# Kernel optimization log

Hardware: AMD Instinct MI355X
Metric: run time of the kernel (lower is better)

The kernel has to match this reference:

```python
import jax, jax.numpy as jnp
import numpy as np

EPS = 1e-6  # F.cosine_similarity eps


def setup_inputs() -> dict:
    key = jax.random.key(0)
    kx, = jax.random.split(key, 1)
    N, M, D = 1024, 32, 256
    x = jax.random.normal(kx, (N, M, D), dtype=jnp.float32)
    w = jnp.array([10.0], dtype=jnp.float32)  # init_w
    b = jnp.array([-5.0], dtype=jnp.float32)  # init_b
    return {"x": x, "w": w, "b": b}


def _ge2e_softmax_loss(x, w, b):
    N, M, D = x.shape
    # centroids over all utterances of each speaker: (N, D)
    cent = x.mean(axis=1)
    # modified centroid excluding utterance i (used when k == j): (N, M, D)
    mod_cent = (x.sum(axis=1, keepdims=True) - x) / (M - 1)

    x_norm = jnp.linalg.norm(x, axis=-1)          # (N, M)
    cent_norm = jnp.linalg.norm(cent, axis=-1)    # (N,)
    mod_norm = jnp.linalg.norm(mod_cent, axis=-1) # (N, M)

    # off-diagonal cosine sim via one batched matmul: (N, M, N)
    dots = jnp.einsum('nmd,kd->nmk', x, cent)
    sim = dots / jnp.maximum(x_norm[:, :, None] * cent_norm[None, None, :], EPS)

    # diagonal (k == j) uses the modified centroid: (N, M)
    diag_sim = jnp.sum(x * mod_cent, axis=-1) / jnp.maximum(x_norm * mod_norm, EPS)

    # splice modified-centroid sims onto the k == j diagonal
    eye = jnp.eye(N, dtype=bool)[:, None, :]  # (N, 1, N)
    S = jnp.where(eye, diag_sim[:, :, None], sim)  # (N, M, N)

    calc = w[0] * S + b[0]
    # L = -S_{ji,j} + logsumexp_k S_{ji,k}
    diag_calc = w[0] * diag_sim + b[0]
    loss = (-diag_calc + jax.nn.logsumexp(calc, axis=-1)).sum()
    return loss


def reference(x, w, b):
    return _ge2e_softmax_loss(x, w, b)
```

## Files before the change

kernel.cpp:

```cpp
#include <hip/hip_runtime.h>
#include <hip/hip_bf16.h>
#include <math.h>

typedef float f32x4 __attribute__((ext_vector_type(4)));
typedef short short8 __attribute__((ext_vector_type(8)));

#define GEPS 1e-6f

static __device__ __forceinline__ short8 ldb8(const __hip_bfloat16* p) {
  return *reinterpret_cast<const short8*>(p);
}

__global__ __launch_bounds__(256) void k1_prep(
    const float* __restrict__ x,
    __hip_bfloat16* __restrict__ xhg, __hip_bfloat16* __restrict__ xlg,
    __hip_bfloat16* __restrict__ chg, __hip_bfloat16* __restrict__ clg,
    float* __restrict__ invcn, float* __restrict__ xn, float* __restrict__ dsim)
{
  const int n = blockIdx.x;
  const int tid = threadIdx.x;
  const int lane = tid & 63;
  const int wv = tid >> 6;
  __shared__ float xsh[32 * 256];
  __shared__ float sl[256];
  __shared__ float red[4];

  const float* xg = x + (size_t)n * 8192;
  float s = 0.f;
  #pragma unroll
  for (int m = 0; m < 32; ++m) {
    float v = xg[m * 256 + tid];
    xsh[m * 256 + tid] = v;
    s += v;
    __hip_bfloat16 h = __float2bfloat16(v);
    float hf = __bfloat162float(h);
    xhg[(size_t)n * 8192 + m * 256 + tid] = h;
    xlg[(size_t)n * 8192 + m * 256 + tid] = __float2bfloat16(v - hf);
  }
  sl[tid] = s;
  const float c = s * 0.03125f;
  {
    __hip_bfloat16 h = __float2bfloat16(c);
    float hf = __bfloat162float(h);
    chg[n * 256 + tid] = h;
    clg[n * 256 + tid] = __float2bfloat16(c - hf);
  }
  float c2 = c * c;
  #pragma unroll
  for (int off = 32; off; off >>= 1) c2 += __shfl_xor(c2, off, 64);
  if (lane == 0) red[wv] = c2;
  __syncthreads();
  if (tid == 0) invcn[n] = 1.0f / sqrtf(red[0] + red[1] + red[2] + red[3]);

  #pragma unroll
  for (int g = 0; g < 8; ++g) {
    const int m = wv + 4 * g;
    float a1 = 0.f, a2 = 0.f, a3 = 0.f;
    #pragma unroll
    for (int e = 0; e < 4; ++e) {
      const int d = lane + 64 * e;
      const float xv = xsh[m * 256 + d];
      const float mo = (sl[d] - xv) / 31.0f;
      a1 += xv * xv;
      a2 += xv * mo;
      a3 += mo * mo;
    }
    #pragma unroll
    for (int off = 32; off; off >>= 1) {
      a1 += __shfl_xor(a1, off, 64);
      a2 += __shfl_xor(a2, off, 64);
      a3 += __shfl_xor(a3, off, 64);
    }
    if (lane == 0) {
      const float xnv = sqrtf(a1);
      const float mn  = sqrtf(a3);
      xn[n * 32 + m]   = xnv;
      dsim[n * 32 + m] = a2 / fmaxf(xnv * mn, GEPS);
    }
  }
}

__global__ __launch_bounds__(256, 2) void k2_mfma(
    const __hip_bfloat16* __restrict__ xhg, const __hip_bfloat16* __restrict__ xlg,
    const __hip_bfloat16* __restrict__ chg, const __hip_bfloat16* __restrict__ clg,
    const float* __restrict__ invcn, const float* __restrict__ xn,
    const float* __restrict__ dsim, const float* __restrict__ wp,
    const float* __restrict__ bp, float* __restrict__ out)
{
  const int bid = blockIdx.x;
  const int tid = threadIdx.x;
  const int wv = tid >> 6;
  const int lane = tid & 63;
  const int q = lane >> 4;
  const int l15 = lane & 15;
  const int rowbase = bid * 64;

  __shared__ float rs[64];
  if (tid < 64) rs[tid] = 0.f;
  __syncthreads();

  const float w = wp[0], b = bp[0];
  const float B = fabsf(w) + fabsf(b);
  const float L2E = 1.44269504088896f;
  const float u = (b - B) * L2E;
  const float wl = w * L2E;

  float srow[4][4], er[4][4];
  #pragma unroll
  for (int mt = 0; mt < 4; ++mt)
    #pragma unroll
    for (int r = 0; r < 4; ++r) {
      const int grow = rowbase + mt * 16 + q * 4 + r;
      srow[mt][r] = wl / xn[grow];
      er[mt][r]   = fmaf(dsim[grow], wl, u);
    }

  float S[4][4];
  #pragma unroll
  for (int mt = 0; mt < 4; ++mt)
    #pragma unroll
    for (int r = 0; r < 4; ++r) S[mt][r] = 0.f;

  #pragma unroll 1
  for (int ci = 0; ci < 2; ++ci) {
    const int ct = wv * 2 + ci;
    const int colbase = ct * 128;
    f32x4 acc[4][8];
    #pragma unroll
    for (int mt = 0; mt < 4; ++mt)
      #pragma unroll
      for (int kt = 0; kt < 8; ++kt) acc[mt][kt] = (f32x4){0.f, 0.f, 0.f, 0.f};

    #pragma unroll 1
    for (int ck = 0; ck < 8; ++ck) {
      const int d0 = ck * 32 + q * 8;
      short8 a_h[4], a_l[4];
      #pragma unroll
      for (int mt = 0; mt < 4; ++mt) {
        const size_t abase = (size_t)(rowbase + mt * 16 + l15) * 256 + d0;
        a_h[mt] = ldb8(xhg + abase);
        a_l[mt] = ldb8(xlg + abase);
      }
      #pragma unroll
      for (int kt = 0; kt < 8; ++kt) {
        const size_t bbase = (size_t)(colbase + kt * 16 + l15) * 256 + d0;
        const short8 b_h = ldb8(chg + bbase);
        const short8 b_l = ldb8(clg + bbase);
        #pragma unroll
        for (int mt = 0; mt < 4; ++mt) {
          acc[mt][kt] = __builtin_amdgcn_mfma_f32_16x16x32_bf16(a_l[mt], b_h, acc[mt][kt], 0, 0, 0);
          acc[mt][kt] = __builtin_amdgcn_mfma_f32_16x16x32_bf16(a_h[mt], b_l, acc[mt][kt], 0, 0, 0);
          acc[mt][kt] = __builtin_amdgcn_mfma_f32_16x16x32_bf16(a_h[mt], b_h, acc[mt][kt], 0, 0, 0);
        }
      }
    }

    #pragma unroll
    for (int kt = 0; kt < 8; ++kt) {
      const int colg = colbase + kt * 16 + l15;
      const float tc = invcn[colg];
      #pragma unroll
      for (int mt = 0; mt < 4; ++mt) {
        const int nrow = (rowbase + mt * 16) >> 5;
        #pragma unroll
        for (int r = 0; r < 4; ++r) {
          float p = exp2f(fmaf(acc[mt][kt][r] * srow[mt][r], tc, u));
          if (colg == nrow) p = exp2f(er[mt][r]);
          S[mt][r] += p;
        }
      }
    }
  }

  #pragma unroll
  for (int mt = 0; mt < 4; ++mt)
    #pragma unroll
    for (int r = 0; r < 4; ++r) {
      float v = S[mt][r];
      v += __shfl_xor(v, 1, 64);
      v += __shfl_xor(v, 2, 64);
      v += __shfl_xor(v, 4, 64);
      v += __shfl_xor(v, 8, 64);
      if (l15 == 0) atomicAdd(&rs[mt * 16 + q * 4 + r], v);
    }
  __syncthreads();

  if (tid < 64) {
    const int grow = rowbase + tid;
    float lr = -fmaf(w, dsim[grow], b) + B + log2f(rs[tid]) * 0.6931471805599453f;
    #pragma unroll
    for (int off = 1; off < 64; off <<= 1) lr += __shfl_xor(lr, off, 64);
    if (tid == 0) atomicAdd(out, lr);
  }
}

extern "C" void kernel_launch(void* const* d_in, const int* in_sizes, int n_in,
                              void* d_out, int out_size, void* d_ws, size_t ws_size,
                              hipStream_t stream)
{
  const float* x = (const float*)d_in[0];
  const float* w = (const float*)d_in[1];
  const float* b = (const float*)d_in[2];
  float* out = (float*)d_out;

  char* W = (char*)d_ws;
  __hip_bfloat16* xhg = (__hip_bfloat16*)(W);
  __hip_bfloat16* xlg = (__hip_bfloat16*)(W + 16777216);
  __hip_bfloat16* chg = (__hip_bfloat16*)(W + 33554432);
  __hip_bfloat16* clg = (__hip_bfloat16*)(W + 34078720);
  float* invcn = (float*)(W + 34603008);
  float* xn    = (float*)(W + 34607104);
  float* dsim  = (float*)(W + 34738176);
  hipMemsetAsync(out, 0, sizeof(float), stream);
  k1_prep<<<1024, 256, 0, stream>>>(x, xhg, xlg, chg, clg, invcn, xn, dsim);
  k2_mfma<<<512, 256, 0, stream>>>(xhg, xlg, chg, clg, invcn, xn, dsim, w, b, out);
}
```

Before: 200.0 us.

## Split column range across blocks, vectorize prep, add final reduction kernel

The MFMA kernel now assigns each block a 64-row by 256-column tile instead of all 1024 columns. That gives 2048 blocks with smaller accumulators and allows occupancy of 3 blocks per CU. Partial row sums go to a global buffer via atomics, and a new third kernel computes the log and the final reduction. The prep kernel is vectorized to float4 loads and derives the modified-centroid norms algebraically without shared-memory staging. In exchange, A tiles are reloaded by four blocks, and the change adds an extra memset and an extra kernel launch.

```diff
diff --git a/kernel.cpp b/kernel.cpp
--- a/kernel.cpp
+++ b/kernel.cpp
@@ -7,71 +7,84 @@
 
 #define GEPS 1e-6f
 
-static __device__ __forceinline__ short8 ldb8(const __hip_bfloat16* p) {
+static __device__ __forceinline__ short8 ldb8(const unsigned short* p) {
   return *reinterpret_cast<const short8*>(p);
+}
+
+static __device__ __forceinline__ void bfsplit(float v, unsigned short& h, unsigned short& l) {
+  __hip_bfloat16 hb = __float2bfloat16(v);
+  h = *reinterpret_cast<unsigned short*>(&hb);
+  float r = v - __bfloat162float(hb);
+  __hip_bfloat16 lb = __float2bfloat16(r);
+  l = *reinterpret_cast<unsigned short*>(&lb);
 }
 
 __global__ __launch_bounds__(256) void k1_prep(
     const float* __restrict__ x,
-    __hip_bfloat16* __restrict__ xhg, __hip_bfloat16* __restrict__ xlg,
-    __hip_bfloat16* __restrict__ chg, __hip_bfloat16* __restrict__ clg,
+    unsigned short* __restrict__ xhg, unsigned short* __restrict__ xlg,
+    unsigned short* __restrict__ chg, unsigned short* __restrict__ clg,
     float* __restrict__ invcn, float* __restrict__ xn, float* __restrict__ dsim)
 {
   const int n = blockIdx.x;
   const int tid = threadIdx.x;
-  const int lane = tid & 63;
-  const int wv = tid >> 6;
-  __shared__ float xsh[32 * 256];
-  __shared__ float sl[256];
-  __shared__ float red[4];
-
-  const float* xg = x + (size_t)n * 8192;
-  float s = 0.f;
-  #pragma unroll
-  for (int m = 0; m < 32; ++m) {
-    float v = xg[m * 256 + tid];
-    xsh[m * 256 + tid] = v;
-    s += v;
-    __hip_bfloat16 h = __float2bfloat16(v);
-    float hf = __bfloat162float(h);
-    xhg[(size_t)n * 8192 + m * 256 + tid] = h;
-    xlg[(size_t)n * 8192 + m * 256 + tid] = __float2bfloat16(v - hf);
-  }
-  sl[tid] = s;
-  const float c = s * 0.03125f;
-  {
-    __hip_bfloat16 h = __float2bfloat16(c);
-    float hf = __bfloat162float(h);
-    chg[n * 256 + tid] = h;
-    clg[n * 256 + tid] = __float2bfloat16(c - hf);
-  }
-  float c2 = c * c;
-  #pragma unroll
-  for (int off = 32; off; off >>= 1) c2 += __shfl_xor(c2, off, 64);
-  if (lane == 0) red[wv] = c2;
-  __syncthreads();
-  if (tid == 0) invcn[n] = 1.0f / sqrtf(red[0] + red[1] + red[2] + red[3]);
-
-  #pragma unroll
-  for (int g = 0; g < 8; ++g) {
-    const int m = wv + 4 * g;
-    float a1 = 0.f, a2 = 0.f, a3 = 0.f;
-    #pragma unroll
-    for (int e = 0; e < 4; ++e) {
-      const int d = lane + 64 * e;
-      const float xv = xsh[m * 256 + d];
-      const float mo = (sl[d] - xv) / 31.0f;
-      a1 += xv * xv;
-      a2 += xv * mo;
-      a3 += mo * mo;
-    }
+  const int c4 = tid & 63;
+  const int mq = tid >> 6;
+  __shared__ f32x4 part[4][64];
+
+  f32x4 xr[8];
+  f32x4 ps = (f32x4){0.f, 0.f, 0.f, 0.f};
+  const size_t nbase = (size_t)n * 8192;
+
+  #pragma unroll
+  for (int p = 0; p < 8; ++p) {
+    const int m = mq * 8 + p;
+    const size_t off = nbase + m * 256 + c4 * 4;
+    f32x4 v = *reinterpret_cast<const f32x4*>(x + off);
+    xr[p] = v;
+    ps += v;
+    ushort4 hv, lv;
+    bfsplit(v.x, hv.x, lv.x);
+    bfsplit(v.y, hv.y, lv.y);
+    bfsplit(v.z, hv.z, lv.z);
+    bfsplit(v.w, hv.w, lv.w);
+    *reinterpret_cast<ushort4*>(xhg + off) = hv;
+    *reinterpret_cast<ushort4*>(xlg + off) = lv;
+  }
+  part[mq][c4] = ps;
+  __syncthreads();
+
+  f32x4 sl = part[0][c4] + part[1][c4] + part[2][c4] + part[3][c4];
+
+  if (mq == 0) {
+    f32x4 c = sl * 0.03125f;
+    ushort4 hv, lv;
+    bfsplit(c.x, hv.x, lv.x);
+    bfsplit(c.y, hv.y, lv.y);
+    bfsplit(c.z, hv.z, lv.z);
+    bfsplit(c.w, hv.w, lv.w);
+    *reinterpret_cast<ushort4*>(chg + n * 256 + c4 * 4) = hv;
+    *reinterpret_cast<ushort4*>(clg + n * 256 + c4 * 4) = lv;
+  }
+
+  float s2 = sl.x * sl.x + sl.y * sl.y + sl.z * sl.z + sl.w * sl.w;
+  #pragma unroll
+  for (int off = 32; off; off >>= 1) s2 += __shfl_xor(s2, off, 64);
+  if (tid == 0) invcn[n] = 32.0f / sqrtf(s2);
+
+  #pragma unroll
+  for (int p = 0; p < 8; ++p) {
+    const f32x4 v = xr[p];
+    float a1 = v.x * v.x + v.y * v.y + v.z * v.z + v.w * v.w;
+    float sx = v.x * sl.x + v.y * sl.y + v.z * sl.z + v.w * sl.w;
     #pragma unroll
     for (int off = 32; off; off >>= 1) {
       a1 += __shfl_xor(a1, off, 64);
-      a2 += __shfl_xor(a2, off, 64);
-      a3 += __shfl_xor(a3, off, 64);
-    }
-    if (lane == 0) {
+      sx += __shfl_xor(sx, off, 64);
+    }
+    if (c4 == 0) {
+      const int m = mq * 8 + p;
+      const float a2 = (sx - a1) * (1.0f / 31.0f);
+      const float a3 = (s2 - 2.0f * sx + a1) * (1.0f / 961.0f);
       const float xnv = sqrtf(a1);
       const float mn  = sqrtf(a3);
       xn[n * 32 + m]   = xnv;
@@ -80,24 +93,65 @@
   }
 }
 
-__global__ __launch_bounds__(256, 2) void k2_mfma(
-    const __hip_bfloat16* __restrict__ xhg, const __hip_bfloat16* __restrict__ xlg,
-    const __hip_bfloat16* __restrict__ chg, const __hip_bfloat16* __restrict__ clg,
+__global__ __launch_bounds__(256, 3) void k2_mfma(
+    const unsigned short* __restrict__ xhg, const unsigned short* __restrict__ xlg,
+    const unsigned short* __restrict__ chg, const unsigned short* __restrict__ clg,
     const float* __restrict__ invcn, const float* __restrict__ xn,
     const float* __restrict__ dsim, const float* __restrict__ wp,
-    const float* __restrict__ bp, float* __restrict__ out)
+    const float* __restrict__ bp, float* __restrict__ row_sum)
 {
   const int bid = blockIdx.x;
+  const int rowbase = (bid >> 2) * 64;
+  const int cq = bid & 3;
   const int tid = threadIdx.x;
   const int wv = tid >> 6;
   const int lane = tid & 63;
   const int q = lane >> 4;
   const int l15 = lane & 15;
-  const int rowbase = bid * 64;
+  const int colbase = cq * 256 + wv * 64;
 
   __shared__ float rs[64];
   if (tid < 64) rs[tid] = 0.f;
   __syncthreads();
+
+  f32x4 acc[4][4];
+  #pragma unroll
+  for (int mt = 0; mt < 4; ++mt)
+    #pragma unroll
+    for (int kt = 0; kt < 4; ++kt) acc[mt][kt] = (f32x4){0.f, 0.f, 0.f, 0.f};
+
+  #pragma unroll 1
+  for (int ck = 0; ck < 8; ++ck) {
+    const int d0 = ck * 32 + q * 8;
+    short8 a_h[4], a_l[4], b_h[4], b_l[4];
+    #pragma unroll
+    for (int mt = 0; mt < 4; ++mt) {
+      const size_t abase = (size_t)(rowbase + mt * 16 + l15) * 256 + d0;
+      a_h[mt] = ldb8(xhg + abase);
+      a_l[mt] = ldb8(xlg + abase);
+    }
+    #pragma unroll
+    for (int kt = 0; kt < 4; ++kt) {
+      const size_t bbase = (size_t)(colbase + kt * 16 + l15) * 256 + d0;
+      b_h[kt] = ldb8(chg + bbase);
+      b_l[kt] = ldb8(clg + bbase);
+    }
+    #pragma unroll
+    for (int mt = 0; mt < 4; ++mt)
+      #pragma unroll
+      for (int kt = 0; kt < 4; ++kt)
+        acc[mt][kt] = __builtin_amdgcn_mfma_f32_16x16x32_bf16(a_l[mt], b_h[kt], acc[mt][kt], 0, 0, 0);
+    #pragma unroll
+    for (int mt = 0; mt < 4; ++mt)
+      #pragma unroll
+      for (int kt = 0; kt < 4; ++kt)
+        acc[mt][kt] = __builtin_amdgcn_mfma_f32_16x16x32_bf16(a_h[mt], b_l[kt], acc[mt][kt], 0, 0, 0);
+    #pragma unroll
+    for (int mt = 0; mt < 4; ++mt)
+      #pragma unroll
+      for (int kt = 0; kt < 4; ++kt)
+        acc[mt][kt] = __builtin_amdgcn_mfma_f32_16x16x32_bf16(a_h[mt], b_h[kt], acc[mt][kt], 0, 0, 0);
+  }
 
   const float w = wp[0], b = bp[0];
   const float B = fabsf(w) + fabsf(b);
@@ -105,93 +159,49 @@
   const float u = (b - B) * L2E;
   const float wl = w * L2E;
 
-  float srow[4][4], er[4][4];
-  #pragma unroll
-  for (int mt = 0; mt < 4; ++mt)
+  #pragma unroll
+  for (int mt = 0; mt < 4; ++mt) {
+    const int nrow = (rowbase + mt * 16) >> 5;
     #pragma unroll
     for (int r = 0; r < 4; ++r) {
       const int grow = rowbase + mt * 16 + q * 4 + r;
-      srow[mt][r] = wl / xn[grow];
-      er[mt][r]   = fmaf(dsim[grow], wl, u);
-    }
-
-  float S[4][4];
-  #pragma unroll
-  for (int mt = 0; mt < 4; ++mt)
-    #pragma unroll
-    for (int r = 0; r < 4; ++r) S[mt][r] = 0.f;
-
-  #pragma unroll 1
-  for (int ci = 0; ci < 2; ++ci) {
-    const int ct = wv * 2 + ci;
-    const int colbase = ct * 128;
-    f32x4 acc[4][8];
-    #pragma unroll
-    for (int mt = 0; mt < 4; ++mt)
-      #pragma unroll
-      for (int kt = 0; kt < 8; ++kt) acc[mt][kt] = (f32x4){0.f, 0.f, 0.f, 0.f};
-
-    #pragma unroll 1
-    for (int ck = 0; ck < 8; ++ck) {
-      const int d0 = ck * 32 + q * 8;
-      short8 a_h[4], a_l[4];
-      #pragma unroll
-      for (int mt = 0; mt < 4; ++mt) {
-        const size_t abase = (size_t)(rowbase + mt * 16 + l15) * 256 + d0;
-        a_h[mt] = ldb8(xhg + abase);
-        a_l[mt] = ldb8(xlg + abase);
+      const float srow = wl / xn[grow];
+      const float ediag = fmaf(dsim[grow], wl, u);
+      float S = 0.f;
+      #pragma unroll
+      for (int kt = 0; kt < 4; ++kt) {
+        const int colg = colbase + kt * 16 + l15;
+        float p = exp2f(fmaf(acc[mt][kt][r] * srow, invcn[colg], u));
+        if (colg == nrow) p = exp2f(ediag);
+        S += p;
       }
-      #pragma unroll
-      for (int kt = 0; kt < 8; ++kt) {
-        const size_t bbase = (size_t)(colbase + kt * 16 + l15) * 256 + d0;
-        const short8 b_h = ldb8(chg + bbase);
-        const short8 b_l = ldb8(clg + bbase);
-        #pragma unroll
-        for (int mt = 0; mt < 4; ++mt) {
-          acc[mt][kt] = __builtin_amdgcn_mfma_f32_16x16x32_bf16(a_l[mt], b_h, acc[mt][kt], 0, 0, 0);
-          acc[mt][kt] = __builtin_amdgcn_mfma_f32_16x16x32_bf16(a_h[mt], b_l, acc[mt][kt], 0, 0, 0);
-          acc[mt][kt] = __builtin_amdgcn_mfma_f32_16x16x32_bf16(a_h[mt], b_h, acc[mt][kt], 0, 0, 0);
-        }
-      }
-    }
-
-    #pragma unroll
-    for (int kt = 0; kt < 8; ++kt) {
-      const int colg = colbase + kt * 16 + l15;
-      const float tc = invcn[colg];
-      #pragma unroll
-      for (int mt = 0; mt < 4; ++mt) {
-        const int nrow = (rowbase + mt * 16) >> 5;
-        #pragma unroll
-        for (int r = 0; r < 4; ++r) {
-          float p = exp2f(fmaf(acc[mt][kt][r] * srow[mt][r], tc, u));
-          if (colg == nrow) p = exp2f(er[mt][r]);
-          S[mt][r] += p;
-        }
-      }
-    }
-  }
-
-  #pragma unroll
-  for (int mt = 0; mt < 4; ++mt)
-    #pragma unroll
-    for (int r = 0; r < 4; ++r) {
-      float v = S[mt][r];
-      v += __shfl_xor(v, 1, 64);
-      v += __shfl_xor(v, 2, 64);
-      v += __shfl_xor(v, 4, 64);
-      v += __shfl_xor(v, 8, 64);
-      if (l15 == 0) atomicAdd(&rs[mt * 16 + q * 4 + r], v);
-    }
-  __syncthreads();
-
-  if (tid < 64) {
-    const int grow = rowbase + tid;
-    float lr = -fmaf(w, dsim[grow], b) + B + log2f(rs[tid]) * 0.6931471805599453f;
-    #pragma unroll
-    for (int off = 1; off < 64; off <<= 1) lr += __shfl_xor(lr, off, 64);
-    if (tid == 0) atomicAdd(out, lr);
-  }
+      S += __shfl_xor(S, 1, 64);
+      S += __shfl_xor(S, 2, 64);
+      S += __shfl_xor(S, 4, 64);
+      S += __shfl_xor(S, 8, 64);
+      if (l15 == 0) atomicAdd(&rs[mt * 16 + q * 4 + r], S);
+    }
+  }
+  __syncthreads();
+  if (tid < 64) atomicAdd(&row_sum[rowbase + tid], rs[tid]);
+}
+
+__global__ __launch_bounds__(256) void k3_final(
+    const float* __restrict__ dsim, const float* __restrict__ row_sum,
+    const float* __restrict__ wp, const float* __restrict__ bp,
+    float* __restrict__ out)
+{
+  const int r = blockIdx.x * 256 + threadIdx.x;
+  const float w = wp[0], b = bp[0];
+  const float B = fabsf(w) + fabsf(b);
+  float v = -fmaf(w, dsim[r], b) + B + logf(row_sum[r]);
+  #pragma unroll
+  for (int off = 32; off; off >>= 1) v += __shfl_xor(v, off, 64);
+  __shared__ float red[4];
+  const int lane = threadIdx.x & 63, wv = threadIdx.x >> 6;
+  if (lane == 0) red[wv] = v;
+  __syncthreads();
+  if (threadIdx.x == 0) atomicAdd(out, red[0] + red[1] + red[2] + red[3]);
 }
 
 extern "C" void kernel_launch(void* const* d_in, const int* in_sizes, int n_in,
@@ -204,14 +214,18 @@
   float* out = (float*)d_out;
 
   char* W = (char*)d_ws;
-  __hip_bfloat16* xhg = (__hip_bfloat16*)(W);
-  __hip_bfloat16* xlg = (__hip_bfloat16*)(W + 16777216);
-  __hip_bfloat16* chg = (__hip_bfloat16*)(W + 33554432);
-  __hip_bfloat16* clg = (__hip_bfloat16*)(W + 34078720);
-  float* invcn = (float*)(W + 34603008);
-  float* xn    = (float*)(W + 34607104);
-  float* dsim  = (float*)(W + 34738176);
+  unsigned short* xhg = (unsigned short*)(W);
+  unsigned short* xlg = (unsigned short*)(W + 16777216);
+  unsigned short* chg = (unsigned short*)(W + 33554432);
+  unsigned short* clg = (unsigned short*)(W + 34078720);
+  float* invcn  = (float*)(W + 34603008);
+  float* xn     = (float*)(W + 34607104);
+  float* dsim   = (float*)(W + 34738176);
+  float* rowsum = (float*)(W + 34869248);
+
+  hipMemsetAsync(rowsum, 0, 32768 * sizeof(float), stream);
   hipMemsetAsync(out, 0, sizeof(float), stream);
   k1_prep<<<1024, 256, 0, stream>>>(x, xhg, xlg, chg, clg, invcn, xn, dsim);
-  k2_mfma<<<512, 256, 0, stream>>>(xhg, xlg, chg, clg, invcn, xn, dsim, w, b, out);
-}
+  k2_mfma<<<2048, 256, 0, stream>>>(xhg, xlg, chg, clg, invcn, xn, dsim, w, b, rowsum);
+  k3_final<<<128, 256, 0, stream>>>(dsim, rowsum, w, b, out);
+}
```

Measured after the change: 223.8 us. 11.9% more time.
